# Kernel optimization log

Hardware: AMD Instinct MI355X
Metric: run time of the kernel (lower is better)

## Reference

```python
import jax, jax.numpy as jnp
import numpy as np

RES_H, RES_W = 64, 64
INV_SMOOTHNESS = 0.1
OFFSET = 0.5
LOSS_WEIGHT = 1.0


def bilinear_sample(mask, xs, ys):
    # mask: [IH, IW]; xs: [Wo]; ys: [Ho] in pixel coords -> [Ho, Wo]
    IH, IW = mask.shape
    x0 = jnp.floor(xs); y0 = jnp.floor(ys)
    wx = xs - x0; wy = ys - y0
    x0i = jnp.clip(x0.astype(jnp.int32), 0, IW - 1)
    x1i = jnp.clip(x0i + 1, 0, IW - 1)
    y0i = jnp.clip(y0.astype(jnp.int32), 0, IH - 1)
    y1i = jnp.clip(y0i + 1, 0, IH - 1)
    g = lambda yi, xi: mask[yi[:, None], xi[None, :]]
    return ((1 - wy)[:, None] * ((1 - wx)[None, :] * g(y0i, x0i) + wx[None, :] * g(y0i, x1i))
            + wy[:, None] * ((1 - wx)[None, :] * g(y1i, x0i) + wx[None, :] * g(y1i, x1i)))


def crop_and_resize(masks, boxes, Ho, Wo):
    # masks: [N, IH, IW]; boxes: [N, 4] xyxy -> binarized [N, Ho, Wo]
    def one(mask, box):
        x1, y1, x2, y2 = box[0], box[1], box[2], box[3]
        xs = x1 + (x2 - x1) * (jnp.arange(Wo, dtype=masks.dtype) + 0.5) / Wo - 0.5
        ys = y1 + (y2 - y1) * (jnp.arange(Ho, dtype=masks.dtype) + 0.5) / Ho - 0.5
        return bilinear_sample(mask, xs, ys)
    out = jax.vmap(one)(masks, boxes)
    return (out >= 0.5).astype(masks.dtype)


def rasterize_mask(verts, H, W, inv_s):
    # Soft polygon rasterization, MODE_MASK: sigmoid(sign * min_sq_dist * inv_s).
    # verts: [N, V, 2] (x, y) in pixel coords of the HxW grid.
    N, V, _ = verts.shape
    xs = jnp.arange(W, dtype=verts.dtype)
    ys = jnp.arange(H, dtype=verts.dtype)
    px = jnp.tile(xs, H)       # [P] with P = H*W
    py = jnp.repeat(ys, W)     # [P]
    p = jnp.stack([px, py], -1)  # [P, 2]
    a = verts                          # [N, V, 2]
    b = jnp.roll(verts, -1, axis=1)    # next vertex (closed polygon)
    ab = b - a                         # [N, V, 2]
    denom = jnp.sum(ab * ab, -1)       # [N, V]
    pa = p[None, :, None, :] - a[:, None, :, :]            # [N, P, V, 2]
    t = jnp.clip(jnp.einsum('npvc,nvc->npv', pa, ab) / (denom[:, None, :] + 1e-12), 0.0, 1.0)
    diff = pa - t[..., None] * ab[:, None, :, :]
    d2 = jnp.sum(diff * diff, -1)      # [N, P, V] squared point-to-segment dist
    d2min = jnp.min(d2, -1)            # [N, P]
    # even-odd crossing test for inside/outside sign
    ay = a[..., 1][:, None, :]; by = b[..., 1][:, None, :]     # [N, 1, V]
    pyb = py[None, :, None]
    cond = (ay > pyb) != (by > pyb)                             # [N, P, V]
    dy = ab[..., 1][:, None, :]
    safe_dy = jnp.where(dy == 0, 1.0, dy)
    xint = a[..., 0][:, None, :] + (pyb - ay) * ab[..., 0][:, None, :] / safe_dy
    crossings = jnp.sum((cond & (px[None, :, None] < xint)).astype(jnp.int32), -1)  # [N, P]
    sign = jnp.where(crossings % 2 == 1, 1.0, -1.0)
    return jax.nn.sigmoid(sign * d2min * inv_s).reshape(N, H, W)


def dice_loss(inp, tgt):
    n = inp.shape[0]
    smooth = 1.0
    iflat = inp.reshape(n, -1)
    tflat = tgt.reshape(n, -1)
    inter = jnp.sum(iflat * tflat, -1)
    losses = 1.0 - (2.0 * inter + smooth) / (jnp.sum(iflat, -1) + jnp.sum(tflat, -1) + smooth)
    return jnp.sum(losses) / n


def setup_inputs() -> dict:
    key = jax.random.key(0)
    k1, k2, k3, k4, k5, k6 = jax.random.split(key, 6)
    N, V, IMG = 128, 128, 512
    # star-shaped polygons (realistic contours) in image coords
    ctr = jax.random.uniform(k1, (N, 1, 2)) * (IMG * 0.6) + IMG * 0.2
    ang = jnp.linspace(0.0, 2.0 * jnp.pi, V, endpoint=False)
    rad = 20.0 + jax.random.uniform(k2, (N, V)) * 60.0
    preds = ctr + jnp.stack([rad * jnp.cos(ang), rad * jnp.sin(ang)], -1)  # [N, V, 2]
    # gt boxes xyxy
    x1y1 = jax.random.uniform(k3, (N, 2)) * (IMG * 0.3)
    wh = 50.0 + jax.random.uniform(k4, (N, 2)) * (IMG * 0.4)
    targets_bboxes = jnp.concatenate([x1y1, x1y1 + wh], -1)  # [N, 4]
    # gt full-image masks: random disks
    cb = jax.random.uniform(k5, (N, 2)) * IMG
    r = 30.0 + jax.random.uniform(k6, (N,)) * 100.0
    yy = jnp.arange(IMG, dtype=jnp.float32)[None, :, None]
    xx = jnp.arange(IMG, dtype=jnp.float32)[None, None, :]
    targets_masks = (((xx - cb[:, 0, None, None]) ** 2 + (yy - cb[:, 1, None, None]) ** 2)
                     < (r[:, None, None] ** 2)).astype(jnp.float32)  # [N, IMG, IMG]
    return {"preds": preds, "targets_masks": targets_masks, "targets_bboxes": targets_bboxes}


def reference(preds, targets_masks, targets_bboxes):
    # union bboxes of predicted polygon extent and gt bbox
    pmin = jnp.min(preds, axis=1)
    pmax = jnp.max(preds, axis=1)
    ub = jnp.concatenate([jnp.minimum(pmin, targets_bboxes[:, :2]),
                          jnp.maximum(pmax, targets_bboxes[:, 2:4])], -1)  # [N, 4]
    # crop + resize + binarize gt masks at the union boxes
    tgt = crop_and_resize(targets_masks, ub, RES_H, RES_W)  # [N, 64, 64]
    # normalize polygons into the (detached) union box
    ubd = jax.lax.stop_gradient(ub)
    normed = (preds - ubd[:, None, :2]) / (ubd[:, None, 2:4] - ubd[:, None, :2])
    verts = normed * float(RES_W) - OFFSET
    pred_masks = rasterize_mask(verts, RES_H, RES_W, INV_SMOOTHNESS)  # [N, 64, 64]
    pred_masks = jnp.clip(pred_masks, 1e-5, 0.99999)
    return dice_loss(pred_masks, tgt) * LOSS_WEIGHT
```

## Files before the change

### kernel.cpp

```cpp
#include <hip/hip_runtime.h>
#include <hip/hip_bf16.h>

#define NMASK 128
#define NV    128
#define IMG   512
#define RES   64
#define PB    8
#define NBLK  (NMASK*PB)
#define BT    256

#define PACC_OFF 0

#define CULL_D2 118.0f

__device__ __forceinline__ int clampi(int v, int lo, int hi) {
    return v < lo ? lo : (v > hi ? hi : v);
}

__device__ __forceinline__ int detect_bf16(const void* preds) {
    const __hip_bfloat16* pb = (const __hip_bfloat16*)preds;
    int lane = threadIdx.x & 63;
    float v = __bfloat162float(pb[2 * lane]);
    bool ok = (v >= 1.0f) && (v <= 600.0f);
    unsigned long long m = __ballot(ok);
    return (m == 0xFFFFFFFFFFFFFFFFULL) ? 1 : 0;
}

__device__ __forceinline__ float loadf(const void* p, long idx, int isb) {
    if (isb) return __bfloat162float(((const __hip_bfloat16*)p)[idx]);
    return ((const float*)p)[idx];
}

__global__ void __launch_bounds__(BT) MaskRasterizationLoss_2705829396671_kernel(
    const void* __restrict__ preds,
    const void* __restrict__ masks,
    const void* __restrict__ bboxes,
    float* __restrict__ pacc)
{
    int n    = blockIdx.x >> 3;
    int part = blockIdx.x & 7;
    int t    = threadIdx.x;
    int lane = t & 63;

    int isb = detect_bf16(preds);

    __shared__ float r[2][4];
    __shared__ float2 vn[NV];
    __shared__ float4 sNA[NV];
    __shared__ float2 sNB[NV];
    __shared__ float4 sCR[NV];
    __shared__ int cnts[2];
    if (t < 2) cnts[t] = 0;

    float vx = 0.0f, vy = 0.0f;
    if (t < NV) {
        vx = loadf(preds, ((long)n*NV + t)*2 + 0, isb);
        vy = loadf(preds, ((long)n*NV + t)*2 + 1, isb);
        float mnx = vx, mxx = vx, mny = vy, mxy = vy;
        for (int off = 32; off >= 1; off >>= 1) {
            mnx = fminf(mnx, __shfl_xor(mnx, off));
            mxx = fmaxf(mxx, __shfl_xor(mxx, off));
            mny = fminf(mny, __shfl_xor(mny, off));
            mxy = fmaxf(mxy, __shfl_xor(mxy, off));
        }
        int w = t >> 6;
        if (lane == 0) { r[w][0]=mnx; r[w][1]=mxx; r[w][2]=mny; r[w][3]=mxy; }
    }
    __syncthreads();
    float mnx = fminf(r[0][0], r[1][0]);
    float mxx = fmaxf(r[0][1], r[1][1]);
    float mny = fminf(r[0][2], r[1][2]);
    float mxy = fmaxf(r[0][3], r[1][3]);

    float bx1 = loadf(bboxes, n*4 + 0, isb);
    float by1 = loadf(bboxes, n*4 + 1, isb);
    float bx2 = loadf(bboxes, n*4 + 2, isb);
    float by2 = loadf(bboxes, n*4 + 3, isb);
    float ux1 = fminf(mnx, bx1), uy1 = fminf(mny, by1);
    float ux2 = fmaxf(mxx, bx2), uy2 = fmaxf(mxy, by2);
    float sx = (float)RES / (ux2 - ux1);
    float sy = (float)RES / (uy2 - uy1);

    if (t < NV) vn[t] = make_float2((vx - ux1)*sx - 0.5f, (vy - uy1)*sy - 0.5f);
    __syncthreads();

    float Ylo = (float)(part * 8);
    float Yhi = (float)(part * 8 + 7);

    if (t < NV) {
        float2 a = vn[t];
        float2 b = vn[(t + 1) & (NV - 1)];
        float abx = b.x - a.x, aby = b.y - a.y;
        float inv = 1.0f / (abx*abx + aby*aby + 1e-12f);
        float slope = abx / ((aby == 0.0f) ? 1.0f : aby);

        float xmn = fminf(a.x, b.x), xmx = fmaxf(a.x, b.x);
        float ymn = fminf(a.y, b.y), ymx = fmaxf(a.y, b.y);

        float dx = fmaxf(fmaxf(xmn - 63.0f, -xmx), 0.0f);
        float dy = fmaxf(fmaxf(ymn - Yhi, Ylo - ymx), 0.0f);
        float lb = fmaf(dx, dx, dy*dy);
        bool keepN = lb < CULL_D2;
        unsigned long long m = __ballot(keepN);
        int pre  = __popcll(m & ((1ull << lane) - 1ull));
        int base = 0;
        if (lane == 0) base = atomicAdd(&cnts[0], (int)__popcll(m));
        base = __shfl(base, 0);
        if (keepN) {
            sNA[base+pre] = make_float4(a.x, a.y, abx, aby);
            sNB[base+pre] = make_float2(abx*inv, aby*inv);
        }

        bool keepC = !((ymn > Yhi) || (ymx <= Ylo));
        m = __ballot(keepC);
        pre = __popcll(m & ((1ull << lane) - 1ull));
        if (lane == 0) base = atomicAdd(&cnts[1], (int)__popcll(m));
        base = __shfl(base, 0);
        if (keepC) sCR[base+pre] = make_float4(a.x, a.y, slope, b.y);
    }
    __syncthreads();
    int nNear  = __builtin_amdgcn_readfirstlane(cnts[0]);
    int nCross = __builtin_amdgcn_readfirstlane(cnts[1]);

    int p0 = part * 512 + t * 2;
    float py  = (float)(p0 >> 6);
    float pxb = (float)(p0 & 63);
    float px1v = pxb + 1.0f;

    float d2m0 = 1e30f, d2m1 = 1e30f;
    int   cr0 = 0, cr1 = 0;

    #pragma unroll 4
    for (int i = 0; i < nNear; ++i) {
        float4 A = sNA[i];
        float2 B = sNB[i];

        float pay  = py - A.y;
        float q    = pay * B.y;
        {
            float pax = pxb - A.x;
            float tt  = fmaf(pax, B.x, q);
            tt = fminf(fmaxf(tt, 0.0f), 1.0f);
            float dx  = fmaf(-tt, A.z, pax);
            float dyv = fmaf(-tt, A.w, pay);
            float d2  = fmaf(dx, dx, dyv*dyv);
            d2m0 = fminf(d2m0, d2);
        }
        {
            float pax = px1v - A.x;
            float tt  = fmaf(pax, B.x, q);
            tt = fminf(fmaxf(tt, 0.0f), 1.0f);
            float dx  = fmaf(-tt, A.z, pax);
            float dyv = fmaf(-tt, A.w, pay);
            float d2  = fmaf(dx, dx, dyv*dyv);
            d2m1 = fminf(d2m1, d2);
        }
    }

    #pragma unroll 4
    for (int i = 0; i < nCross; ++i) {
        float4 C = sCR[i];

        float pay  = py - C.y;
        bool  cnd  = (C.y > py) != (C.w > py);
        float xint = fmaf(pay, C.z, C.x);
        cr0 += (cnd && (pxb  < xint)) ? 1 : 0;
        cr1 += (cnd && (px1v < xint)) ? 1 : 0;
    }

    long mbase = (long)n * IMG * IMG;
    float invW = (ux2 - ux1) * (1.0f/(float)RES);
    float invH = (uy2 - uy1) * (1.0f/(float)RES);
    float ys = fmaf(py + 0.5f, invH, uy1) - 0.5f;
    float fy = floorf(ys), wy = ys - fy;
    int y0i = clampi((int)fy, 0, IMG-1);
    int y1i = clampi(y0i + 1, 0, IMG-1);

    float s_pred = 0.0f, s_tgt = 0.0f, s_int = 0.0f;
    #pragma unroll
    for (int k = 0; k < 2; ++k) {
        float px    = k ? px1v : pxb;
        float d2min = k ? d2m1 : d2m0;
        int   cross = k ? cr1  : cr0;

        float sgn = (cross & 1) ? 1.0f : -1.0f;
        float z = sgn * d2min * 0.1f;
        float sg = 1.0f / (1.0f + __expf(-z));
        sg = fminf(fmaxf(sg, 1e-5f), 0.99999f);

        float xs = fmaf(px + 0.5f, invW, ux1) - 0.5f;
        float fx = floorf(xs), wx = xs - fx;
        int x0i = clampi((int)fx, 0, IMG-1);
        int x1i = clampi(x0i + 1, 0, IMG-1);
        float g00 = loadf(masks, mbase + (long)y0i*IMG + x0i, isb);
        float g01 = loadf(masks, mbase + (long)y0i*IMG + x1i, isb);
        float g10 = loadf(masks, mbase + (long)y1i*IMG + x0i, isb);
        float g11 = loadf(masks, mbase + (long)y1i*IMG + x1i, isb);
        float bil = (1.0f-wy) * ((1.0f-wx)*g00 + wx*g01)
                  +        wy * ((1.0f-wx)*g10 + wx*g11);
        float tg = (bil >= 0.5f) ? 1.0f : 0.0f;

        s_pred += sg;
        s_tgt  += tg;
        s_int  += sg * tg;
    }

    for (int off = 32; off >= 1; off >>= 1) {
        s_pred += __shfl_xor(s_pred, off);
        s_tgt  += __shfl_xor(s_tgt,  off);
        s_int  += __shfl_xor(s_int,  off);
    }
    __shared__ float red[3][4];
    int wave = t >> 6;
    if ((t & 63) == 0) { red[0][wave]=s_pred; red[1][wave]=s_tgt; red[2][wave]=s_int; }
    __syncthreads();
    if (t == 0) {
        pacc[blockIdx.x*3+0] = red[0][0]+red[0][1]+red[0][2]+red[0][3];
        pacc[blockIdx.x*3+1] = red[1][0]+red[1][1]+red[1][2]+red[1][3];
        pacc[blockIdx.x*3+2] = red[2][0]+red[2][1]+red[2][2]+red[2][3];
    }
}

__global__ void __launch_bounds__(128) finalize_kernel(
    const float* __restrict__ pacc, void* __restrict__ out)
{
    int t = threadIdx.x;
    float sp = 0.0f, st = 0.0f, si = 0.0f;
    #pragma unroll
    for (int p = 0; p < PB; ++p) {
        sp += pacc[(t*PB + p)*3 + 0];
        st += pacc[(t*PB + p)*3 + 1];
        si += pacc[(t*PB + p)*3 + 2];
    }
    float loss = 1.0f - (2.0f*si + 1.0f) / (sp + st + 1.0f);
    for (int off = 32; off >= 1; off >>= 1)
        loss += __shfl_xor(loss, off);
    __shared__ float tmp[2];
    if ((t & 63) == 0) tmp[t >> 6] = loss;
    __syncthreads();
    if (t == 0) {
        float L = (tmp[0] + tmp[1]) * (1.0f/128.0f);
        unsigned int fb = __float_as_uint(L);
        unsigned int r  = (fb + 0x7FFFu + ((fb >> 16) & 1u)) >> 16;
        ((unsigned int*)out)[0] = (r << 16) | r;
    }
}

extern "C" void kernel_launch(void* const* d_in, const int* in_sizes, int n_in,
                              void* d_out, int out_size, void* d_ws, size_t ws_size,
                              hipStream_t stream) {
    const void* preds  = d_in[0];
    const void* masks  = d_in[1];
    const void* bboxes = d_in[2];
    float* ws = (float*)d_ws;

    MaskRasterizationLoss_2705829396671_kernel<<<NBLK, BT, 0, stream>>>(
        preds, masks, bboxes, ws + PACC_OFF);
    finalize_kernel<<<1, 128, 0, stream>>>(ws + PACC_OFF, d_out);
}
```

Measured before the change: 181.9 us.

## Build per-wave near-segment lists over 16x8 pixel tiles for tighter culling

Each wave now covers a 16-column by 8-row tile instead of two full rows, and builds its own culled near-segment list using that tile's x-range, so fewer segments survive the distance bound per wave. The cross-edge list is built by wave 0 alone, and the shared atomic counters give way to per-wave ballot prefix counts. The aim is to cut the inner distance-loop trip count. The cost is redundant edge scans in every wave and more shared memory.

```diff
diff --git a/kernel.cpp b/kernel.cpp
--- a/kernel.cpp
+++ b/kernel.cpp
@@ -41,16 +41,16 @@
     int part = blockIdx.x & 7;
     int t    = threadIdx.x;
     int lane = t & 63;
+    int w    = t >> 6;
 
     int isb = detect_bf16(preds);
 
     __shared__ float r[2][4];
     __shared__ float2 vn[NV];
-    __shared__ float4 sNA[NV];
-    __shared__ float2 sNB[NV];
+    __shared__ float4 sNA[4][NV];
+    __shared__ float2 sNB[4][NV];
     __shared__ float4 sCR[NV];
-    __shared__ int cnts[2];
-    if (t < 2) cnts[t] = 0;
+    __shared__ int nCrossS;
 
     float vx = 0.0f, vy = 0.0f;
     if (t < NV) {
@@ -63,7 +63,6 @@
             mny = fminf(mny, __shfl_xor(mny, off));
             mxy = fmaxf(mxy, __shfl_xor(mxy, off));
         }
-        int w = t >> 6;
         if (lane == 0) { r[w][0]=mnx; r[w][1]=mxx; r[w][2]=mny; r[w][3]=mxy; }
     }
     __syncthreads();
@@ -86,45 +85,58 @@
 
     float Ylo = (float)(part * 8);
     float Yhi = (float)(part * 8 + 7);
-
-    if (t < NV) {
-        float2 a = vn[t];
-        float2 b = vn[(t + 1) & (NV - 1)];
+    float X0f = (float)(16 * w);
+    float X1f = X0f + 15.0f;
+    unsigned long long llt = (1ull << lane) - 1ull;
+
+    int nNear = 0;
+    #pragma unroll
+    for (int rnd = 0; rnd < 2; ++rnd) {
+        int e = rnd*64 + lane;
+        float2 a = vn[e];
+        float2 b = vn[(e + 1) & (NV - 1)];
         float abx = b.x - a.x, aby = b.y - a.y;
-        float inv = 1.0f / (abx*abx + aby*aby + 1e-12f);
-        float slope = abx / ((aby == 0.0f) ? 1.0f : aby);
-
         float xmn = fminf(a.x, b.x), xmx = fmaxf(a.x, b.x);
         float ymn = fminf(a.y, b.y), ymx = fmaxf(a.y, b.y);
-
-        float dx = fmaxf(fmaxf(xmn - 63.0f, -xmx), 0.0f);
+        float dx = fmaxf(fmaxf(xmn - X1f, X0f - xmx), 0.0f);
         float dy = fmaxf(fmaxf(ymn - Yhi, Ylo - ymx), 0.0f);
         float lb = fmaf(dx, dx, dy*dy);
-        bool keepN = lb < CULL_D2;
-        unsigned long long m = __ballot(keepN);
-        int pre  = __popcll(m & ((1ull << lane) - 1ull));
-        int base = 0;
-        if (lane == 0) base = atomicAdd(&cnts[0], (int)__popcll(m));
-        base = __shfl(base, 0);
-        if (keepN) {
-            sNA[base+pre] = make_float4(a.x, a.y, abx, aby);
-            sNB[base+pre] = make_float2(abx*inv, aby*inv);
-        }
-
-        bool keepC = !((ymn > Yhi) || (ymx <= Ylo));
-        m = __ballot(keepC);
-        pre = __popcll(m & ((1ull << lane) - 1ull));
-        if (lane == 0) base = atomicAdd(&cnts[1], (int)__popcll(m));
-        base = __shfl(base, 0);
-        if (keepC) sCR[base+pre] = make_float4(a.x, a.y, slope, b.y);
-    }
-    __syncthreads();
-    int nNear  = __builtin_amdgcn_readfirstlane(cnts[0]);
-    int nCross = __builtin_amdgcn_readfirstlane(cnts[1]);
-
-    int p0 = part * 512 + t * 2;
-    float py  = (float)(p0 >> 6);
-    float pxb = (float)(p0 & 63);
+        bool keep = lb < CULL_D2;
+        unsigned long long m = __ballot(keep);
+        if (keep) {
+            int p = nNear + (int)__popcll(m & llt);
+            sNA[w][p] = make_float4(a.x, a.y, abx, aby);
+            float inv = 1.0f / (abx*abx + aby*aby + 1e-12f);
+            sNB[w][p] = make_float2(abx*inv, aby*inv);
+        }
+        nNear += (int)__popcll(m);
+    }
+
+    if (w == 0) {
+        int cnt = 0;
+        #pragma unroll
+        for (int rnd = 0; rnd < 2; ++rnd) {
+            int e = rnd*64 + lane;
+            float2 a = vn[e];
+            float2 b = vn[(e + 1) & (NV - 1)];
+            float ymn = fminf(a.y, b.y), ymx = fmaxf(a.y, b.y);
+            bool keep = !((ymn > Yhi) || (ymx <= Ylo));
+            unsigned long long m = __ballot(keep);
+            if (keep) {
+                int p = cnt + (int)__popcll(m & llt);
+                float abx = b.x - a.x, aby = b.y - a.y;
+                float slope = abx / ((aby == 0.0f) ? 1.0f : aby);
+                sCR[p] = make_float4(a.x, a.y, slope, b.y);
+            }
+            cnt += (int)__popcll(m);
+        }
+        if (lane == 0) nCrossS = cnt;
+    }
+    __syncthreads();
+    int nCross = __builtin_amdgcn_readfirstlane(nCrossS);
+
+    float py   = (float)(part*8 + (lane >> 3));
+    float pxb  = (float)(16*w + 2*(lane & 7));
     float px1v = pxb + 1.0f;
 
     float d2m0 = 1e30f, d2m1 = 1e30f;
@@ -132,8 +144,8 @@
 
     #pragma unroll 4
     for (int i = 0; i < nNear; ++i) {
-        float4 A = sNA[i];
-        float2 B = sNB[i];
+        float4 A = sNA[w][i];
+        float2 B = sNB[w][i];
 
         float pay  = py - A.y;
         float q    = pay * B.y;
@@ -211,8 +223,7 @@
         s_int  += __shfl_xor(s_int,  off);
     }
     __shared__ float red[3][4];
-    int wave = t >> 6;
-    if ((t & 63) == 0) { red[0][wave]=s_pred; red[1][wave]=s_tgt; red[2][wave]=s_int; }
+    if (lane == 0) { red[0][w]=s_pred; red[1][w]=s_tgt; red[2][w]=s_int; }
     __syncthreads();
     if (t == 0) {
         pacc[blockIdx.x*3+0] = red[0][0]+red[0][1]+red[0][2]+red[0][3];
```

Measured after the change: 179.1 us. About the same (-1.5%).
